# Performance work log

Hardware: AMD Instinct MI355X
Metric: run time of the kernel (lower is better)

## Reference

```python
import jax, jax.numpy as jnp
import numpy as np

S = 2048      # max_seq_len
D_IN = 2048   # input dim
H = 16        # num query heads
KVH = 4       # kv heads (GQA branch)
HD = 128      # per-head embedding dim
D_OUT = 2048
THETA = 10000.0


def rope(x):
    # x: [S, h, d]. Matches eqx.nn.RotaryPositionalEmbedding (GPT-NeoX style):
    # cos/sin of outer(t, inv_freq) tiled over the two halves, rotate_half = (-x2, x1).
    s, h, d = x.shape
    inv_freq = 1.0 / (THETA ** (jnp.arange(0, d, 2, dtype=jnp.float32) / d))  # [d/2]
    t = jnp.arange(s, dtype=jnp.float32)
    freqs = jnp.outer(t, inv_freq)                         # [S, d/2]
    cos = jnp.tile(jnp.cos(freqs), (1, 2))[:, None, :]     # [S, 1, d]
    sin = jnp.tile(jnp.sin(freqs), (1, 2))[:, None, :]
    x1, x2 = jnp.split(x, 2, axis=-1)
    rot = jnp.concatenate((-x2, x1), axis=-1)
    return x * cos + rot * sin


def setup_inputs() -> dict:
    key = jax.random.key(0)
    k0, k1, k2, k3, k4 = jax.random.split(key, 5)
    lim_in = 1.0 / np.sqrt(D_IN).astype(np.float32)
    lim_o = 1.0 / np.sqrt(H * HD).astype(np.float32)
    x = jax.random.normal(k0, (S, D_IN), jnp.float32)
    Wq = jax.random.uniform(k1, (H * HD, D_IN), jnp.float32, -lim_in, lim_in)
    Wk = jax.random.uniform(k2, (KVH * HD, D_IN), jnp.float32, -lim_in, lim_in)
    Wv = jax.random.uniform(k3, (KVH * HD, D_IN), jnp.float32, -lim_in, lim_in)
    Wo = jax.random.uniform(k4, (D_OUT, H * HD), jnp.float32, -lim_o, lim_o)
    return {"x": x, "Wq": Wq, "Wk": Wk, "Wv": Wv, "Wo": Wo}


def reference(x, Wq, Wk, Wv, Wo):
    # Projections (eqx Linear, no bias: y = W @ x)
    q = (x @ Wq.T).reshape(S, H, HD)
    k = (x @ Wk.T).reshape(S, KVH, HD)
    v = (x @ Wv.T).reshape(S, KVH, HD)
    q = rope(q)
    k = rope(k)
    mask = jnp.tril(jnp.ones((S, S), dtype=bool))           # causal
    scale = 1.0 / jnp.sqrt(jnp.asarray(HD, q.dtype))
    # GQA branch: every query head attends against every kv head separately
    logits = jnp.einsum('shd,SHd->hHsS', q * scale, k)      # [H=16, KVH=4, S, S]
    logits = jnp.where(mask, logits, jnp.finfo(logits.dtype).min)
    w = jax.nn.softmax(logits, axis=-1)
    attn = jnp.einsum('hHsS,SHd->shd', w, v) / KVH          # mean over kv heads
    return attn.reshape(S, H * HD) @ Wo.T
```

## Files before the change

### kernel.cpp

```cpp
#include <hip/hip_runtime.h>

#define SEQ 2048
#define DIN 2048
#define NH 16
#define NKVH 4
#define DH 128
#define NQ 2048
#define QSCALE 0.088388347648318447f

typedef unsigned short ushort_t;
typedef unsigned int uint_t;
typedef __attribute__((ext_vector_type(8))) __bf16 bf16x8;
typedef __attribute__((ext_vector_type(8))) unsigned short ushort8;
typedef __attribute__((ext_vector_type(4))) float f32x4;
typedef __attribute__((ext_vector_type(16))) float f32x16;

__device__ __forceinline__ float b2f(ushort_t u){ return __uint_as_float(((unsigned int)u)<<16); }
__device__ __forceinline__ ushort_t f2b(float f){
  unsigned int u = __float_as_uint(f);
  u += 0x7fff + ((u>>16)&1);
  return (ushort_t)(u>>16);
}
__device__ __forceinline__ f32x4 mfma16(bf16x8 a, bf16x8 b, f32x4 c){
  return __builtin_amdgcn_mfma_f32_16x16x32_bf16(a, b, c, 0, 0, 0);
}
__device__ __forceinline__ f32x16 mfma32(bf16x8 a, bf16x8 b, f32x16 c){
  return __builtin_amdgcn_mfma_f32_32x32x16_bf16(a, b, c, 0, 0, 0);
}
__device__ __forceinline__ void gload16(const void* g, void* l){
  __builtin_amdgcn_global_load_lds((__attribute__((address_space(1))) void*)(void*)g,
                                   (__attribute__((address_space(3))) void*)l, 16, 0, 0);
}
__device__ __forceinline__ f32x16 zero16(){
  f32x16 z = {0.f,0.f,0.f,0.f,0.f,0.f,0.f,0.f,0.f,0.f,0.f,0.f,0.f,0.f,0.f,0.f};
  return z;
}

__global__ void detect_bf16(const ushort_t* __restrict__ wq, int* __restrict__ flag){
  __shared__ int any_big;
  if (threadIdx.x==0) any_big = 0;
  __syncthreads();
  int big = 0;
  for (int i=threadIdx.x; i<4096; i+=256){
    float v = b2f(wq[i]);
    if (!(fabsf(v) < 1.0f)) big = 1;
  }
  if (big) atomicOr(&any_big, 1);
  __syncthreads();
  if (threadIdx.x==0) flag[0] = any_big ? 0 : 1;
}

__global__ __launch_bounds__(256)
void cvt_bf16(const void* __restrict__ src, ushort_t* __restrict__ dst,
              const int* __restrict__ flag){
  const int i = (blockIdx.x*256 + threadIdx.x)*8;
  if (flag[0]){
    *(ushort8*)&dst[i] = *(const ushort8*)((const ushort_t*)src + i);
  } else {
    f32x4 a = *(const f32x4*)((const float*)src + i);
    f32x4 b = *(const f32x4*)((const float*)src + i + 4);
    ushort8 w;
    #pragma unroll
    for (int e=0;e<4;e++){ w[e]=f2b(a[e]); w[4+e]=f2b(b[e]); }
    *(ushort8*)&dst[i] = w;
  }
}

__global__ __launch_bounds__(256)
void sum4(const ushort_t* __restrict__ pb, ushort_t* __restrict__ ab){
  const size_t PS = (size_t)SEQ*NQ;
  const int i = (blockIdx.x*256 + threadIdx.x)*8;
  ushort8 a = *(const ushort8*)&pb[i];
  ushort8 b = *(const ushort8*)&pb[PS + i];
  ushort8 c = *(const ushort8*)&pb[2*PS + i];
  ushort8 d = *(const ushort8*)&pb[3*PS + i];
  ushort8 w;
  #pragma unroll
  for (int e=0;e<8;e++)
    w[e] = f2b((b2f(a[e]) + b2f(b[e])) + (b2f(c[e]) + b2f(d[e])));
  *(ushort8*)&ab[i] = w;
}

__device__ __forceinline__ void stage128x32(const ushort_t* src, int ld, char* ldsbase, int tid){
  #pragma unroll
  for (int p=0;p<2;p++){
    int lin = p*4096 + tid*16;
    int r = lin>>6, cb = lin&63;
    gload16(src + (size_t)r*ld + (cb>>1), ldsbase + p*4096 + ((tid>>6)<<10));
  }
}

__global__ __launch_bounds__(256, 2)
void gemm_qkv(const ushort_t* __restrict__ X, const ushort_t* __restrict__ Wq,
              const ushort_t* __restrict__ Wk, const ushort_t* __restrict__ Wv,
              ushort_t* __restrict__ qb, ushort_t* __restrict__ kb,
              ushort_t* __restrict__ vb){
  __shared__ __attribute__((aligned(16))) ushort_t lds_a[2][128*32];
  __shared__ __attribute__((aligned(16))) ushort_t lds_b[2][128*32];
  const int tid = threadIdx.x;
  const int wid = tid>>6, lane = tid&63;
  const int lhi = lane>>4, llo = lane&15;
  const int flat = blockIdx.x + 16*blockIdx.y;
  const int wf = (flat & 7)*48 + (flat >> 3);
  const int mb = (wf & 15)*128;
  const int ny = wf >> 4;
  const ushort_t* W = (ny < 16) ? (Wq + (size_t)ny*128*DIN)
                    : (ny < 20) ? (Wk + (size_t)(ny-16)*128*DIN)
                    : (Wv + (size_t)(ny-20)*128*DIN);
  const int wr = (wid>>1)*64, wc = (wid&1)*64;

  f32x4 acc[4][4];
  #pragma unroll
  for (int i=0;i<4;i++)
    #pragma unroll
    for (int j=0;j<4;j++) acc[i][j] = (f32x4){0.f,0.f,0.f,0.f};

  auto stage = [&](int b, int t){
    stage128x32(X + (size_t)mb*DIN + t*32, DIN, (char*)lds_a[b], tid);
    stage128x32(W + t*32, DIN, (char*)lds_b[b], tid);
  };

  stage(0, 0);
  __syncthreads();
  int cur = 0;
  for (int t=0; t<64; ++t){
    if (t < 63) stage(cur^1, t+1);
    bf16x8 af[4], bfr[4];
    #pragma unroll
    for (int i=0;i<4;i++) af[i]  = *(const bf16x8*)&lds_a[cur][(wr+i*16+llo)*32 + lhi*8];
    #pragma unroll
    for (int j=0;j<4;j++) bfr[j] = *(const bf16x8*)&lds_b[cur][(wc+j*16+llo)*32 + lhi*8];
    __builtin_amdgcn_s_setprio(1);
    #pragma unroll
    for (int i=0;i<4;i++)
      #pragma unroll
      for (int j=0;j<4;j++)
        acc[i][j] = mfma16(af[i], bfr[j], acc[i][j]);
    __builtin_amdgcn_s_setprio(0);
    __syncthreads();
    cur ^= 1;
  }
  #pragma unroll
  for (int i=0;i<4;i++)
    #pragma unroll
    for (int j=0;j<4;j++)
      #pragma unroll
      for (int rr=0;rr<4;rr++){
        int s  = mb + wr + i*16 + lhi*4 + rr;
        int nl = wc + j*16 + llo;
        ushort_t val = f2b(acc[i][j][rr]);
        if (ny < 16)      qb[(size_t)s*NQ + ny*128 + nl] = val;
        else if (ny < 20) kb[(size_t)(ny-16)*SEQ*DH + (size_t)s*DH + nl] = val;
        else              vb[(size_t)(ny-20)*SEQ*DH + (size_t)s*DH + nl] = val;
      }
}

__global__ __launch_bounds__(256, 2)
void gemm_plain_b16(const ushort_t* __restrict__ A, const ushort_t* __restrict__ Wo,
                    void* __restrict__ out, const int* __restrict__ flag){
  __shared__ __attribute__((aligned(16))) ushort_t lds_a[2][128*32];
  __shared__ __attribute__((aligned(16))) ushort_t lds_b[2][128*32];
  const int isb = flag[0];
  const int tid = threadIdx.x;
  const int wid = tid>>6, lane = tid&63;
  const int lhi = lane>>4, llo = lane&15;
  const int flat = blockIdx.x + 16*blockIdx.y;
  const int wf = (flat & 7)*32 + (flat >> 3);
  const int mb = (wf & 15)*128;
  const int nb = (wf >> 4)*128;
  const int wr = (wid>>1)*64, wc = (wid&1)*64;

  f32x4 acc[4][4];
  #pragma unroll
  for (int i=0;i<4;i++)
    #pragma unroll
    for (int j=0;j<4;j++) acc[i][j] = (f32x4){0.f,0.f,0.f,0.f};

  auto stage = [&](int b, int t){
    stage128x32(A  + (size_t)mb*NQ + t*32, NQ, (char*)lds_a[b], tid);
    stage128x32(Wo + (size_t)nb*NQ + t*32, NQ, (char*)lds_b[b], tid);
  };

  stage(0, 0);
  __syncthreads();
  int cur = 0;
  for (int t=0; t<64; ++t){
    if (t < 63) stage(cur^1, t+1);
    bf16x8 af[4], bfr[4];
    #pragma unroll
    for (int i=0;i<4;i++) af[i]  = *(const bf16x8*)&lds_a[cur][(wr+i*16+llo)*32 + lhi*8];
    #pragma unroll
    for (int j=0;j<4;j++) bfr[j] = *(const bf16x8*)&lds_b[cur][(wc+j*16+llo)*32 + lhi*8];
    __builtin_amdgcn_s_setprio(1);
    #pragma unroll
    for (int i=0;i<4;i++)
      #pragma unroll
      for (int j=0;j<4;j++)
        acc[i][j] = mfma16(af[i], bfr[j], acc[i][j]);
    __builtin_amdgcn_s_setprio(0);
    __syncthreads();
    cur ^= 1;
  }
  #pragma unroll
  for (int i=0;i<4;i++)
    #pragma unroll
    for (int j=0;j<4;j++)
      #pragma unroll
      for (int rr=0;rr<4;rr++){
        int s  = mb + wr + i*16 + lhi*4 + rr;
        int nl = nb + wc + j*16 + llo;
        float v = acc[i][j][rr];
        if (isb) ((ushort_t*)out)[(size_t)s*NQ + nl] = f2b(v);
        else     ((float*)out)[(size_t)s*NQ + nl] = v;
      }
}

__global__ __launch_bounds__(256, 2)
void gemm_plain_f32(const float* __restrict__ A, const ushort_t* __restrict__ Wo,
                    void* __restrict__ out, const int* __restrict__ flag){
  __shared__ __attribute__((aligned(16))) ushort_t lds_a[2][128*32];
  __shared__ __attribute__((aligned(16))) ushort_t lds_b[2][128*32];
  const int isb = flag[0];
  const int tid = threadIdx.x;
  const int wid = tid>>6, lane = tid&63;
  const int lhi = lane>>4, llo = lane&15;
  const int mb = blockIdx.x*128;
  const int nb = blockIdx.y*128;
  const int wr = (wid>>1)*64, wc = (wid&1)*64;
  const int r = tid>>1, c0 = (tid&1)*16;
  const float* Ab = A + (size_t)(mb+r)*NQ + c0;

  f32x4 acc[4][4];
  #pragma unroll
  for (int i=0;i<4;i++)
    #pragma unroll
    for (int j=0;j<4;j++) acc[i][j] = (f32x4){0.f,0.f,0.f,0.f};

  f32x4 raf[4];
  auto ldA = [&](int t){
    raf[0] = *(const f32x4*)(Ab + t*32);
    raf[1] = *(const f32x4*)(Ab + t*32 + 4);
    raf[2] = *(const f32x4*)(Ab + t*32 + 8);
    raf[3] = *(const f32x4*)(Ab + t*32 + 12);
  };
  auto stA = [&](ushort_t* lds){
    ushort8 w0, w1;
    #pragma unroll
    for (int e=0;e<4;e++){ w0[e]=f2b(raf[0][e]); w0[4+e]=f2b(raf[1][e]);
                           w1[e]=f2b(raf[2][e]); w1[4+e]=f2b(raf[3][e]); }
    *(ushort8*)&lds[r*32+c0]   = w0;
    *(ushort8*)&lds[r*32+c0+8] = w1;
  };

  ldA(0);
  stage128x32(Wo + (size_t)nb*NQ, NQ, (char*)lds_b[0], tid);
  stA(lds_a[0]);
  __syncthreads();
  int cur = 0;
  for (int t=0; t<64; ++t){
    const bool more = (t < 63);
    if (more){
      ldA(t+1);
      stage128x32(Wo + (size_t)nb*NQ + (t+1)*32, NQ, (char*)lds_b[cur^1], tid);
    }
    bf16x8 af[4], bfr[4];
    #pragma unroll
    for (int i=0;i<4;i++) af[i]  = *(const bf16x8*)&lds_a[cur][(wr+i*16+llo)*32 + lhi*8];
    #pragma unroll
    for (int j=0;j<4;j++) bfr[j] = *(const bf16x8*)&lds_b[cur][(wc+j*16+llo)*32 + lhi*8];
    __builtin_amdgcn_s_setprio(1);
    #pragma unroll
    for (int i=0;i<4;i++)
      #pragma unroll
      for (int j=0;j<4;j++)
        acc[i][j] = mfma16(af[i], bfr[j], acc[i][j]);
    __builtin_amdgcn_s_setprio(0);
    if (more) stA(lds_a[cur^1]);
    __syncthreads();
    cur ^= 1;
  }
  #pragma unroll
  for (int i=0;i<4;i++)
    #pragma unroll
    for (int j=0;j<4;j++)
      #pragma unroll
      for (int rr=0;rr<4;rr++){
        int s  = mb + wr + i*16 + lhi*4 + rr;
        int nl = nb + wc + j*16 + llo;
        float v = acc[i][j][rr];
        if (isb) ((ushort_t*)out)[(size_t)s*NQ + nl] = f2b(v);
        else     ((float*)out)[(size_t)s*NQ + nl] = v;
      }
}

__global__ __launch_bounds__(256)
void rope_kernel(ushort_t* __restrict__ buf, int head_stride, int row_stride, float scale){
  const int idx = blockIdx.x*256 + threadIdx.x;
  const int j = idx & 63;
  const int s = (idx>>6) & (SEQ-1);
  const int h = idx>>17;
  const size_t a1 = (size_t)h*head_stride + (size_t)s*row_stride + j;
  const size_t a2 = a1 + 64;
  const float inv = __expf((float)j * -0.1439115683f);
  const float ang = (float)s * inv;
  const float c = cosf(ang), sn = sinf(ang);
  const float x1 = b2f(buf[a1]), x2 = b2f(buf[a2]);
  buf[a1] = f2b((x1*c - x2*sn)*scale);
  buf[a2] = f2b((x2*c + x1*sn)*scale);
}

__global__ __launch_bounds__(256)
void vtrans(const ushort_t* __restrict__ vb, ushort_t* __restrict__ vt){
  __shared__ __attribute__((aligned(16))) ushort_t tile[64*72];
  const int tid = threadIdx.x;
  const int kv = blockIdx.z, s0 = blockIdx.x*64, d0 = blockIdx.y*64;
  #pragma unroll
  for (int p=0;p<2;p++){
    int lin = p*4096 + tid*16;
    int rr = lin>>7, cb = lin&127;
    ushort8 val = *(const ushort8*)&vb[(size_t)kv*SEQ*DH + (size_t)(s0+rr)*DH + d0 + (cb>>1)];
    *(ushort8*)&tile[rr*72 + (cb>>1)] = val;
  }
  __syncthreads();
  #pragma unroll
  for (int p=0;p<2;p++){
    int lin = p*4096 + tid*16;
    int rr = lin>>7, cb = lin&127;
    int cc = cb>>1;
    ushort8 val;
    #pragma unroll
    for (int e=0;e<8;e++) val[e] = tile[(cc+e)*72 + rr];
    *(ushort8*)&vt[(size_t)kv*DH*SEQ + (size_t)(d0+rr)*SEQ + s0 + cc] = val;
  }
}

__global__ __launch_bounds__(256, 2)
void attn_kernel(const ushort_t* __restrict__ qb, const ushort_t* __restrict__ kb,
                 const ushort_t* __restrict__ vt, float* __restrict__ abf,
                 ushort_t* __restrict__ pb, int use_pb){
  __shared__ __attribute__((aligned(16))) ushort_t lds_k[2][64*128];
  __shared__ __attribute__((aligned(16))) ushort_t lds_v[2][128*64];
  __shared__ float lsum[4][32];
  const int tid = threadIdx.x;
  const int wid = tid>>6, lane = tid&63;
  const int l31 = lane&31, hi = lane>>5;
  const int flat = (int)(blockIdx.x + 8*blockIdx.y + 128*blockIdx.z);
  const int xcd = flat & 7, slot = flat >> 3;
  const int kv = xcd >> 1;
  const int ph = (xcd & 1)*64 + slot;
  const int p = ph & 7, h = ph >> 3;
  const ushort_t* kbase = kb + (size_t)kv*SEQ*DH;
  const ushort_t* vbase = vt + (size_t)kv*DH*SEQ;
  const int NKT0 = 2*p + 2;

  auto stage = [&](int b, int kt){
    #pragma unroll
    for (int pp=0;pp<4;pp++){
      int lin = pp*4096 + tid*16;
      int rk = lin>>8, cbk = lin&255;
      int sck = cbk ^ ((rk&15)<<4);
      gload16(kbase + (size_t)(kt*64 + rk)*DH + (sck>>1), (char*)lds_k[b] + pp*4096 + (wid<<10));
      int rv = lin>>7, cbv = lin&127;
      int scv = cbv ^ ((rv&7)<<4);
      gload16(vbase + (size_t)rv*SEQ + kt*64 + (scv>>1), (char*)lds_v[b] + pp*4096 + (wid<<10));
    }
  };

  int sub = 0, kt = 0, t = p;
  int qrow0 = t*128 + wid*32;
  int qg = qrow0 + l31;
  bf16x8 qf[8];
  {
    const ushort_t* qp = qb + (size_t)qg*NQ + h*DH + hi*8;
    #pragma unroll
    for (int ks=0;ks<8;ks++) qf[ks] = *(const bf16x8*)(qp + ks*16);
  }
  f32x16 oacc[4];
  #pragma unroll
  for (int d=0;d<4;d++) oacc[d] = zero16();
  float psum = 0.f;

  stage(0, 0);
  __syncthreads();
  int cur = 0;

  for (int s=0; s<34; ++s){
    {
      int ns = s + 1;
      if (ns < 34) stage(cur^1, ns < NKT0 ? ns : ns - NKT0);
    }
    #pragma unroll
    for (int ss=0;ss<2;ss++){
      const int kvb = kt*64 + ss*32;
      if (kvb > qrow0 + 31) continue;
      f32x16 sacc = zero16();
      #pragma unroll
      for (int ks=0;ks<8;ks++){
        int row = ss*32 + l31;
        int boff = row*256 + ((ks*32 + hi*16) ^ ((row&15)<<4));
        bf16x8 kf = *(const bf16x8*)((const char*)lds_k[cur] + boff);
        sacc = mfma32(kf, qf[ks], sacc);
      }
      const bool edge = (kvb + 31 > qrow0);
      #pragma unroll
      for (int rr=0; rr<16; rr++){
        float e = __expf(sacc[rr]);
        if (edge){
          int kvg = kvb + (rr&3) + 8*(rr>>2) + 4*hi;
          if (kvg > qg) e = 0.f;
        }
        sacc[rr] = e;
        psum += e;
      }
      #pragma unroll
      for (int pk=0; pk<2; pk++){
        uint_t P0, P1, P2, P3;
        asm("v_cvt_pk_bf16_f32 %0, %1, %2" : "=v"(P0) : "v"(sacc[8*pk+0]), "v"(sacc[8*pk+1]));
        asm("v_cvt_pk_bf16_f32 %0, %1, %2" : "=v"(P1) : "v"(sacc[8*pk+2]), "v"(sacc[8*pk+3]));
        asm("v_cvt_pk_bf16_f32 %0, %1, %2" : "=v"(P2) : "v"(sacc[8*pk+4]), "v"(sacc[8*pk+5]));
        asm("v_cvt_pk_bf16_f32 %0, %1, %2" : "=v"(P3) : "v"(sacc[8*pk+6]), "v"(sacc[8*pk+7]));
        asm("v_permlane32_swap_b32 %0, %1" : "+v"(P0), "+v"(P2));
        asm("v_permlane32_swap_b32 %0, %1" : "+v"(P1), "+v"(P3));
        uint4 fu; fu.x = P0; fu.y = P1; fu.z = P2; fu.w = P3;
        bf16x8 pf = *(bf16x8*)&fu;
        #pragma unroll
        for (int d=0; d<4; d++){
          int rowv = d*32 + l31;
          int bv = rowv*128 + ((ss*64 + pk*32 + hi*16) ^ ((rowv&7)<<4));
          bf16x8 vf = *(const bf16x8*)((const char*)lds_v[cur] + bv);
          oacc[d] = mfma32(pf, vf, oacc[d]);
        }
      }
    }
    const int NKTc = sub ? (34 - NKT0) : NKT0;
    if (kt == NKTc - 1){
      float tot = psum + __shfl_xor(psum, 32);
      lsum[wid][l31] = tot;
      if (use_pb){
        ushort_t* pbk = pb + (size_t)kv*SEQ*NQ + (size_t)h*DH;
        #pragma unroll
        for (int rr=0; rr<16; rr++){
          int qr = (rr&3) + 8*(rr>>2) + 4*hi;
          float sc = 0.25f / lsum[wid][qr];
          #pragma unroll
          for (int d=0; d<4; d++)
            pbk[(size_t)(qrow0 + qr)*NQ + d*32 + l31] = f2b(oacc[d][rr]*sc);
        }
      } else {
        #pragma unroll
        for (int rr=0; rr<16; rr++){
          int qr = (rr&3) + 8*(rr>>2) + 4*hi;
          float sc = 0.25f / lsum[wid][qr];
          #pragma unroll
          for (int d=0; d<4; d++)
            atomicAdd(&abf[(size_t)(qrow0 + qr)*NQ + h*DH + d*32 + l31], oacc[d][rr]*sc);
        }
      }
      if (sub == 0){
        sub = 1; kt = 0; t = 15 - p;
        qrow0 = t*128 + wid*32; qg = qrow0 + l31;
        const ushort_t* qp = qb + (size_t)qg*NQ + h*DH + hi*8;
        #pragma unroll
        for (int ks=0;ks<8;ks++) qf[ks] = *(const bf16x8*)(qp + ks*16);
        #pragma unroll
        for (int d=0;d<4;d++) oacc[d] = zero16();
        psum = 0.f;
      }
    } else {
      kt++;
    }
    __syncthreads();
    cur ^= 1;
  }
}

extern "C" void kernel_launch(void* const* d_in, const int* in_sizes, int n_in,
                              void* d_out, int out_size, void* d_ws, size_t ws_size,
                              hipStream_t stream) {
  const void* x  = d_in[0];
  const void* wq = d_in[1];
  const void* wk = d_in[2];
  const void* wv = d_in[3];
  const void* wo = d_in[4];
  char* ws = (char*)d_ws;
  const bool big_ws = (ws_size >= ((size_t)55<<20));

  if (big_ws){
    ushort_t* qbuf = (ushort_t*)(ws);
    ushort_t* kbuf = (ushort_t*)(ws + ((size_t)8<<20));
    ushort_t* vbuf = (ushort_t*)(ws + ((size_t)10<<20));
    ushort_t* vtb  = (ushort_t*)(ws + ((size_t)12<<20));
    ushort_t* pbuf = (ushort_t*)(ws + ((size_t)14<<20));
    ushort_t* xb   = (ushort_t*)(ws + ((size_t)14<<20));
    ushort_t* wqb  = (ushort_t*)(ws + ((size_t)22<<20));
    ushort_t* wkb  = (ushort_t*)(ws + ((size_t)30<<20));
    ushort_t* wvb  = (ushort_t*)(ws + ((size_t)32<<20));
    ushort_t* wob  = (ushort_t*)(ws + ((size_t)46<<20));
    ushort_t* ab   = qbuf;
    int* flag      = (int*)(ws + ((size_t)54<<20));

    hipLaunchKernelGGL(detect_bf16, dim3(1), dim3(256), 0, stream, (const ushort_t*)wq, flag);
    hipLaunchKernelGGL(cvt_bf16, dim3(2048), dim3(256), 0, stream, x,  xb,  flag);
    hipLaunchKernelGGL(cvt_bf16, dim3(2048), dim3(256), 0, stream, wq, wqb, flag);
    hipLaunchKernelGGL(cvt_bf16, dim3(512),  dim3(256), 0, stream, wk, wkb, flag);
    hipLaunchKernelGGL(cvt_bf16, dim3(512),  dim3(256), 0, stream, wv, wvb, flag);
    hipLaunchKernelGGL(cvt_bf16, dim3(2048), dim3(256), 0, stream, wo, wob, flag);
    hipLaunchKernelGGL(gemm_qkv, dim3(16,24), dim3(256), 0, stream, xb, wqb, wkb, wvb, qbuf, kbuf, vbuf);
    hipLaunchKernelGGL(rope_kernel, dim3(8192), dim3(256), 0, stream, qbuf, DH, NQ, QSCALE);
    hipLaunchKernelGGL(rope_kernel, dim3(2048), dim3(256), 0, stream, kbuf, SEQ*DH, DH, 1.0f);
    hipLaunchKernelGGL(vtrans, dim3(32,2,4), dim3(256), 0, stream, vbuf, vtb);
    hipLaunchKernelGGL(attn_kernel, dim3(8,16,4), dim3(256), 0, stream, qbuf, kbuf, vtb,
                       (float*)nullptr, pbuf, 1);
    hipLaunchKernelGGL(sum4, dim3(2048), dim3(256), 0, stream, pbuf, ab);
    hipLaunchKernelGGL(gemm_plain_b16, dim3(16,16), dim3(256), 0, stream, ab, wob, d_out, flag);
  } else {
    ushort_t* qbuf = (ushort_t*)(ws);
    ushort_t* kbuf = (ushort_t*)(ws + ((size_t)8<<20));
    ushort_t* vbuf = (ushort_t*)(ws + ((size_t)10<<20));
    ushort_t* vtb  = (ushort_t*)(ws + ((size_t)12<<20));
    float*    abf  = (float*)(ws + ((size_t)14<<20));
    ushort_t* xb   = (ushort_t*)(ws + ((size_t)14<<20));
    ushort_t* wqb  = (ushort_t*)(ws + ((size_t)22<<20));
    ushort_t* wkb  = (ushort_t*)(ws + ((size_t)30<<20));
    ushort_t* wvb  = (ushort_t*)(ws + ((size_t)32<<20));
    ushort_t* wob  = (ushort_t*)(ws + ((size_t)34<<20));
    int* flag      = (int*)(ws + ((size_t)42<<20));

    hipLaunchKernelGGL(detect_bf16, dim3(1), dim3(256), 0, stream, (const ushort_t*)wq, flag);
    hipLaunchKernelGGL(cvt_bf16, dim3(2048), dim3(256), 0, stream, x,  xb,  flag);
    hipLaunchKernelGGL(cvt_bf16, dim3(2048), dim3(256), 0, stream, wq, wqb, flag);
    hipLaunchKernelGGL(cvt_bf16, dim3(512),  dim3(256), 0, stream, wk, wkb, flag);
    hipLaunchKernelGGL(cvt_bf16, dim3(512),  dim3(256), 0, stream, wv, wvb, flag);
    hipLaunchKernelGGL(cvt_bf16, dim3(2048), dim3(256), 0, stream, wo, wob, flag);
    hipLaunchKernelGGL(gemm_qkv, dim3(16,24), dim3(256), 0, stream, xb, wqb, wkb, wvb, qbuf, kbuf, vbuf);
    hipMemsetAsync(abf, 0, (size_t)SEQ*NQ*sizeof(float), stream);
    hipLaunchKernelGGL(rope_kernel, dim3(8192), dim3(256), 0, stream, qbuf, DH, NQ, QSCALE);
    hipLaunchKernelGGL(rope_kernel, dim3(2048), dim3(256), 0, stream, kbuf, SEQ*DH, DH, 1.0f);
    hipLaunchKernelGGL(vtrans, dim3(32,2,4), dim3(256), 0, stream, vbuf, vtb);
    hipLaunchKernelGGL(attn_kernel, dim3(8,16,4), dim3(256), 0, stream, qbuf, kbuf, vtb,
                       abf, (ushort_t*)nullptr, 0);
    hipLaunchKernelGGL(gemm_plain_f32, dim3(16,16), dim3(256), 0, stream, abf, wob, d_out, flag);
  }
}
```

Baseline: 219.0 us.

## Fuse conversion and rope launches, shrink GEMM tiles, simplify attention to one tile per block

Folds the five conversion launches into one cvt_all kernel and the two rope launches into one rope_all, which cuts launch overhead. Halves the GEMM tile in one dimension (QKV uses 64x128, the output projection 128x64) so more blocks fill the CUs, and raises QKV occupancy to 3 blocks per CU. The attention kernel drops the paired-tile double-buffered pipeline for one query tile per block with single-buffered LDS, ordered to balance causal work, at 4 blocks per CU. It also folds log2(e) into the Q scale so exp2 can replace expf. These changes trade lost load/compute overlap in attention and less per-block reuse in the GEMMs for more parallelism and fewer launches.

```diff
diff --git a/kernel.cpp b/kernel.cpp
--- a/kernel.cpp
+++ b/kernel.cpp
@@ -6,7 +6,7 @@
 #define NKVH 4
 #define DH 128
 #define NQ 2048
-#define QSCALE 0.088388347648318447f
+#define QSCALE2 0.1275174684f
 
 typedef unsigned short ushort_t;
 typedef unsigned int uint_t;
@@ -14,6 +14,12 @@
 typedef __attribute__((ext_vector_type(8))) unsigned short ushort8;
 typedef __attribute__((ext_vector_type(4))) float f32x4;
 typedef __attribute__((ext_vector_type(16))) float f32x16;
+
+#if __has_builtin(__builtin_amdgcn_exp2f)
+#define EXP2(x) __builtin_amdgcn_exp2f(x)
+#else
+#define EXP2(x) exp2f(x)
+#endif
 
 __device__ __forceinline__ float b2f(ushort_t u){ return __uint_as_float(((unsigned int)u)<<16); }
 __device__ __forceinline__ ushort_t f2b(float f){
@@ -51,17 +57,28 @@
 }
 
 __global__ __launch_bounds__(256)
-void cvt_bf16(const void* __restrict__ src, ushort_t* __restrict__ dst,
-              const int* __restrict__ flag){
-  const int i = (blockIdx.x*256 + threadIdx.x)*8;
+void cvt_all(const void* __restrict__ x, const void* __restrict__ wq,
+             const void* __restrict__ wk, const void* __restrict__ wv,
+             const void* __restrict__ wo,
+             ushort_t* __restrict__ xb, ushort_t* __restrict__ wqb,
+             ushort_t* __restrict__ wkb, ushort_t* __restrict__ wvb,
+             ushort_t* __restrict__ wob, const int* __restrict__ flag){
+  int b = blockIdx.x;
+  const void* src; ushort_t* dst; int off;
+  if      (b < 2048){ src=x;  dst=xb;  off=b; }
+  else if (b < 4096){ src=wq; dst=wqb; off=b-2048; }
+  else if (b < 4608){ src=wk; dst=wkb; off=b-4096; }
+  else if (b < 5120){ src=wv; dst=wvb; off=b-4608; }
+  else              { src=wo; dst=wob; off=b-5120; }
+  const int i = (off*256 + threadIdx.x)*8;
   if (flag[0]){
     *(ushort8*)&dst[i] = *(const ushort8*)((const ushort_t*)src + i);
   } else {
     f32x4 a = *(const f32x4*)((const float*)src + i);
-    f32x4 b = *(const f32x4*)((const float*)src + i + 4);
+    f32x4 c = *(const f32x4*)((const float*)src + i + 4);
     ushort8 w;
     #pragma unroll
-    for (int e=0;e<4;e++){ w[e]=f2b(a[e]); w[4+e]=f2b(b[e]); }
+    for (int e=0;e<4;e++){ w[e]=f2b(a[e]); w[4+e]=f2b(c[e]); }
     *(ushort8*)&dst[i] = w;
   }
 }
@@ -89,34 +106,39 @@
     gload16(src + (size_t)r*ld + (cb>>1), ldsbase + p*4096 + ((tid>>6)<<10));
   }
 }
-
-__global__ __launch_bounds__(256, 2)
+__device__ __forceinline__ void stage64x32(const ushort_t* src, int ld, char* ldsbase, int tid){
+  int lin = tid*16;
+  int r = lin>>6, cb = lin&63;
+  gload16(src + (size_t)r*ld + (cb>>1), ldsbase + ((tid>>6)<<10));
+}
+
+__global__ __launch_bounds__(256, 3)
 void gemm_qkv(const ushort_t* __restrict__ X, const ushort_t* __restrict__ Wq,
               const ushort_t* __restrict__ Wk, const ushort_t* __restrict__ Wv,
               ushort_t* __restrict__ qb, ushort_t* __restrict__ kb,
               ushort_t* __restrict__ vb){
-  __shared__ __attribute__((aligned(16))) ushort_t lds_a[2][128*32];
+  __shared__ __attribute__((aligned(16))) ushort_t lds_a[2][64*32];
   __shared__ __attribute__((aligned(16))) ushort_t lds_b[2][128*32];
   const int tid = threadIdx.x;
   const int wid = tid>>6, lane = tid&63;
   const int lhi = lane>>4, llo = lane&15;
-  const int flat = blockIdx.x + 16*blockIdx.y;
-  const int wf = (flat & 7)*48 + (flat >> 3);
-  const int mb = (wf & 15)*128;
-  const int ny = wf >> 4;
+  const int flat = blockIdx.x;
+  const int wf = (flat & 7)*96 + (flat >> 3);
+  const int mb = (wf & 31)*64;
+  const int ny = wf >> 5;
   const ushort_t* W = (ny < 16) ? (Wq + (size_t)ny*128*DIN)
                     : (ny < 20) ? (Wk + (size_t)(ny-16)*128*DIN)
                     : (Wv + (size_t)(ny-20)*128*DIN);
-  const int wr = (wid>>1)*64, wc = (wid&1)*64;
-
-  f32x4 acc[4][4];
-  #pragma unroll
-  for (int i=0;i<4;i++)
+  const int wr = (wid>>1)*32, wc = (wid&1)*64;
+
+  f32x4 acc[2][4];
+  #pragma unroll
+  for (int i=0;i<2;i++)
     #pragma unroll
     for (int j=0;j<4;j++) acc[i][j] = (f32x4){0.f,0.f,0.f,0.f};
 
   auto stage = [&](int b, int t){
-    stage128x32(X + (size_t)mb*DIN + t*32, DIN, (char*)lds_a[b], tid);
+    stage64x32 (X + (size_t)mb*DIN + t*32, DIN, (char*)lds_a[b], tid);
     stage128x32(W + t*32, DIN, (char*)lds_b[b], tid);
   };
 
@@ -125,14 +147,14 @@
   int cur = 0;
   for (int t=0; t<64; ++t){
     if (t < 63) stage(cur^1, t+1);
-    bf16x8 af[4], bfr[4];
-    #pragma unroll
-    for (int i=0;i<4;i++) af[i]  = *(const bf16x8*)&lds_a[cur][(wr+i*16+llo)*32 + lhi*8];
+    bf16x8 af[2], bfr[4];
+    #pragma unroll
+    for (int i=0;i<2;i++) af[i]  = *(const bf16x8*)&lds_a[cur][(wr+i*16+llo)*32 + lhi*8];
     #pragma unroll
     for (int j=0;j<4;j++) bfr[j] = *(const bf16x8*)&lds_b[cur][(wc+j*16+llo)*32 + lhi*8];
     __builtin_amdgcn_s_setprio(1);
     #pragma unroll
-    for (int i=0;i<4;i++)
+    for (int i=0;i<2;i++)
       #pragma unroll
       for (int j=0;j<4;j++)
         acc[i][j] = mfma16(af[i], bfr[j], acc[i][j]);
@@ -141,7 +163,7 @@
     cur ^= 1;
   }
   #pragma unroll
-  for (int i=0;i<4;i++)
+  for (int i=0;i<2;i++)
     #pragma unroll
     for (int j=0;j<4;j++)
       #pragma unroll
@@ -159,26 +181,26 @@
 void gemm_plain_b16(const ushort_t* __restrict__ A, const ushort_t* __restrict__ Wo,
                     void* __restrict__ out, const int* __restrict__ flag){
   __shared__ __attribute__((aligned(16))) ushort_t lds_a[2][128*32];
-  __shared__ __attribute__((aligned(16))) ushort_t lds_b[2][128*32];
+  __shared__ __attribute__((aligned(16))) ushort_t lds_b[2][64*32];
   const int isb = flag[0];
   const int tid = threadIdx.x;
   const int wid = tid>>6, lane = tid&63;
   const int lhi = lane>>4, llo = lane&15;
-  const int flat = blockIdx.x + 16*blockIdx.y;
-  const int wf = (flat & 7)*32 + (flat >> 3);
+  const int flat = blockIdx.x;
+  const int wf = (flat & 7)*64 + (flat >> 3);
   const int mb = (wf & 15)*128;
-  const int nb = (wf >> 4)*128;
-  const int wr = (wid>>1)*64, wc = (wid&1)*64;
-
-  f32x4 acc[4][4];
+  const int nb = (wf >> 4)*64;
+  const int wr = (wid>>1)*64, wc = (wid&1)*32;
+
+  f32x4 acc[4][2];
   #pragma unroll
   for (int i=0;i<4;i++)
     #pragma unroll
-    for (int j=0;j<4;j++) acc[i][j] = (f32x4){0.f,0.f,0.f,0.f};
+    for (int j=0;j<2;j++) acc[i][j] = (f32x4){0.f,0.f,0.f,0.f};
 
   auto stage = [&](int b, int t){
     stage128x32(A  + (size_t)mb*NQ + t*32, NQ, (char*)lds_a[b], tid);
-    stage128x32(Wo + (size_t)nb*NQ + t*32, NQ, (char*)lds_b[b], tid);
+    stage64x32 (Wo + (size_t)nb*NQ + t*32, NQ, (char*)lds_b[b], tid);
   };
 
   stage(0, 0);
@@ -186,16 +208,16 @@
   int cur = 0;
   for (int t=0; t<64; ++t){
     if (t < 63) stage(cur^1, t+1);
-    bf16x8 af[4], bfr[4];
+    bf16x8 af[4], bfr[2];
     #pragma unroll
     for (int i=0;i<4;i++) af[i]  = *(const bf16x8*)&lds_a[cur][(wr+i*16+llo)*32 + lhi*8];
     #pragma unroll
-    for (int j=0;j<4;j++) bfr[j] = *(const bf16x8*)&lds_b[cur][(wc+j*16+llo)*32 + lhi*8];
+    for (int j=0;j<2;j++) bfr[j] = *(const bf16x8*)&lds_b[cur][(wc+j*16+llo)*32 + lhi*8];
     __builtin_amdgcn_s_setprio(1);
     #pragma unroll
     for (int i=0;i<4;i++)
       #pragma unroll
-      for (int j=0;j<4;j++)
+      for (int j=0;j<2;j++)
         acc[i][j] = mfma16(af[i], bfr[j], acc[i][j]);
     __builtin_amdgcn_s_setprio(0);
     __syncthreads();
@@ -204,7 +226,7 @@
   #pragma unroll
   for (int i=0;i<4;i++)
     #pragma unroll
-    for (int j=0;j<4;j++)
+    for (int j=0;j<2;j++)
       #pragma unroll
       for (int rr=0;rr<4;rr++){
         int s  = mb + wr + i*16 + lhi*4 + rr;
@@ -294,8 +316,11 @@
 }
 
 __global__ __launch_bounds__(256)
-void rope_kernel(ushort_t* __restrict__ buf, int head_stride, int row_stride, float scale){
-  const int idx = blockIdx.x*256 + threadIdx.x;
+void rope_all(ushort_t* __restrict__ qbuf, ushort_t* __restrict__ kbuf){
+  int idx = blockIdx.x*256 + threadIdx.x;
+  ushort_t* buf; int head_stride, row_stride; float scale;
+  if (idx < 16*SEQ*64){ buf=qbuf; head_stride=DH; row_stride=NQ; scale=QSCALE2; }
+  else { idx -= 16*SEQ*64; buf=kbuf; head_stride=SEQ*DH; row_stride=DH; scale=1.0f; }
   const int j = idx & 63;
   const int s = (idx>>6) & (SEQ-1);
   const int h = idx>>17;
@@ -334,61 +359,53 @@
   }
 }
 
-__global__ __launch_bounds__(256, 2)
+__global__ __launch_bounds__(256, 4)
 void attn_kernel(const ushort_t* __restrict__ qb, const ushort_t* __restrict__ kb,
                  const ushort_t* __restrict__ vt, float* __restrict__ abf,
                  ushort_t* __restrict__ pb, int use_pb){
-  __shared__ __attribute__((aligned(16))) ushort_t lds_k[2][64*128];
-  __shared__ __attribute__((aligned(16))) ushort_t lds_v[2][128*64];
+  __shared__ __attribute__((aligned(16))) ushort_t lds_k[64*128];
+  __shared__ __attribute__((aligned(16))) ushort_t lds_v[128*64];
   __shared__ float lsum[4][32];
   const int tid = threadIdx.x;
   const int wid = tid>>6, lane = tid&63;
   const int l31 = lane&31, hi = lane>>5;
-  const int flat = (int)(blockIdx.x + 8*blockIdx.y + 128*blockIdx.z);
+  const int flat = (int)(blockIdx.x + 16*blockIdx.y + 256*blockIdx.z);
   const int xcd = flat & 7, slot = flat >> 3;
   const int kv = xcd >> 1;
-  const int ph = (xcd & 1)*64 + slot;
-  const int p = ph & 7, h = ph >> 3;
+  const int idx = slot*2 + (xcd & 1);
+  const int g = idx >> 4, h = idx & 15;
+  const int t = (g<4) ? 15-g : (g<8) ? 4+g : (g<12) ? g-4 : 15-g;
   const ushort_t* kbase = kb + (size_t)kv*SEQ*DH;
   const ushort_t* vbase = vt + (size_t)kv*DH*SEQ;
-  const int NKT0 = 2*p + 2;
-
-  auto stage = [&](int b, int kt){
+  const int NKT = 2*t + 2;
+  const int qrow0 = t*128 + wid*32;
+  const int qg = qrow0 + l31;
+
+  bf16x8 qf[8];
+  {
+    const ushort_t* qp = qb + (size_t)qg*NQ + h*DH + hi*8;
+    #pragma unroll
+    for (int ks=0;ks<8;ks++) qf[ks] = *(const bf16x8*)(qp + ks*16);
+  }
+  f32x16 oacc[4];
+  #pragma unroll
+  for (int d=0;d<4;d++) oacc[d] = zero16();
+  float psum = 0.f;
+
+  for (int kt=0; kt<NKT; ++kt){
+    __syncthreads();
     #pragma unroll
     for (int pp=0;pp<4;pp++){
       int lin = pp*4096 + tid*16;
       int rk = lin>>8, cbk = lin&255;
       int sck = cbk ^ ((rk&15)<<4);
-      gload16(kbase + (size_t)(kt*64 + rk)*DH + (sck>>1), (char*)lds_k[b] + pp*4096 + (wid<<10));
+      gload16(kbase + (size_t)(kt*64 + rk)*DH + (sck>>1), (char*)lds_k + pp*4096 + (wid<<10));
       int rv = lin>>7, cbv = lin&127;
       int scv = cbv ^ ((rv&7)<<4);
-      gload16(vbase + (size_t)rv*SEQ + kt*64 + (scv>>1), (char*)lds_v[b] + pp*4096 + (wid<<10));
+      gload16(vbase + (size_t)rv*SEQ + kt*64 + (scv>>1), (char*)lds_v + pp*4096 + (wid<<10));
     }
-  };
-
-  int sub = 0, kt = 0, t = p;
-  int qrow0 = t*128 + wid*32;
-  int qg = qrow0 + l31;
-  bf16x8 qf[8];
-  {
-    const ushort_t* qp = qb + (size_t)qg*NQ + h*DH + hi*8;
-    #pragma unroll
-    for (int ks=0;ks<8;ks++) qf[ks] = *(const bf16x8*)(qp + ks*16);
-  }
-  f32x16 oacc[4];
-  #pragma unroll
-  for (int d=0;d<4;d++) oacc[d] = zero16();
-  float psum = 0.f;
-
-  stage(0, 0);
-  __syncthreads();
-  int cur = 0;
-
-  for (int s=0; s<34; ++s){
-    {
-      int ns = s + 1;
-      if (ns < 34) stage(cur^1, ns < NKT0 ? ns : ns - NKT0);
-    }
+    __syncthreads();
+
     #pragma unroll
     for (int ss=0;ss<2;ss++){
       const int kvb = kt*64 + ss*32;
@@ -398,13 +415,13 @@
       for (int ks=0;ks<8;ks++){
         int row = ss*32 + l31;
         int boff = row*256 + ((ks*32 + hi*16) ^ ((row&15)<<4));
-        bf16x8 kf = *(const bf16x8*)((const char*)lds_k[cur] + boff);
+        bf16x8 kf = *(const bf16x8*)((const char*)lds_k + boff);
         sacc = mfma32(kf, qf[ks], sacc);
       }
       const bool edge = (kvb + 31 > qrow0);
       #pragma unroll
       for (int rr=0; rr<16; rr++){
-        float e = __expf(sacc[rr]);
+        float e = EXP2(sacc[rr]);
         if (edge){
           int kvg = kvb + (rr&3) + 8*(rr>>2) + 4*hi;
           if (kvg > qg) e = 0.f;
@@ -427,50 +444,36 @@
         for (int d=0; d<4; d++){
           int rowv = d*32 + l31;
           int bv = rowv*128 + ((ss*64 + pk*32 + hi*16) ^ ((rowv&7)<<4));
-          bf16x8 vf = *(const bf16x8*)((const char*)lds_v[cur] + bv);
+          bf16x8 vf = *(const bf16x8*)((const char*)lds_v + bv);
           oacc[d] = mfma32(pf, vf, oacc[d]);
         }
       }
     }
-    const int NKTc = sub ? (34 - NKT0) : NKT0;
-    if (kt == NKTc - 1){
-      float tot = psum + __shfl_xor(psum, 32);
-      lsum[wid][l31] = tot;
-      if (use_pb){
-        ushort_t* pbk = pb + (size_t)kv*SEQ*NQ + (size_t)h*DH;
+  }
+
+  {
+    float tot = psum + __shfl_xor(psum, 32);
+    lsum[wid][l31] = tot;
+    if (use_pb){
+      ushort_t* pbk = pb + (size_t)kv*SEQ*NQ + (size_t)h*DH;
+      #pragma unroll
+      for (int rr=0; rr<16; rr++){
+        int qr = (rr&3) + 8*(rr>>2) + 4*hi;
+        float sc = 0.25f / lsum[wid][qr];
         #pragma unroll
-        for (int rr=0; rr<16; rr++){
-          int qr = (rr&3) + 8*(rr>>2) + 4*hi;
-          float sc = 0.25f / lsum[wid][qr];
-          #pragma unroll
-          for (int d=0; d<4; d++)
-            pbk[(size_t)(qrow0 + qr)*NQ + d*32 + l31] = f2b(oacc[d][rr]*sc);
-        }
-      } else {
+        for (int d=0; d<4; d++)
+          pbk[(size_t)(qrow0 + qr)*NQ + d*32 + l31] = f2b(oacc[d][rr]*sc);
+      }
+    } else {
+      #pragma unroll
+      for (int rr=0; rr<16; rr++){
+        int qr = (rr&3) + 8*(rr>>2) + 4*hi;
+        float sc = 0.25f / lsum[wid][qr];
         #pragma unroll
-        for (int rr=0; rr<16; rr++){
-          int qr = (rr&3) + 8*(rr>>2) + 4*hi;
-          float sc = 0.25f / lsum[wid][qr];
-          #pragma unroll
-          for (int d=0; d<4; d++)
-            atomicAdd(&abf[(size_t)(qrow0 + qr)*NQ + h*DH + d*32 + l31], oacc[d][rr]*sc);
-        }
-      }
-      if (sub == 0){
-        sub = 1; kt = 0; t = 15 - p;
-        qrow0 = t*128 + wid*32; qg = qrow0 + l31;
-        const ushort_t* qp = qb + (size_t)qg*NQ + h*DH + hi*8;
-        #pragma unroll
-        for (int ks=0;ks<8;ks++) qf[ks] = *(const bf16x8*)(qp + ks*16);
-        #pragma unroll
-        for (int d=0;d<4;d++) oacc[d] = zero16();
-        psum = 0.f;
-      }
-    } else {
-      kt++;
+        for (int d=0; d<4; d++)
+          atomicAdd(&abf[(size_t)(qrow0 + qr)*NQ + h*DH + d*32 + l31], oacc[d][rr]*sc);
+      }
     }
-    __syncthreads();
-    cur ^= 1;
   }
 }
 
@@ -500,19 +503,15 @@
     int* flag      = (int*)(ws + ((size_t)54<<20));
 
     hipLaunchKernelGGL(detect_bf16, dim3(1), dim3(256), 0, stream, (const ushort_t*)wq, flag);
-    hipLaunchKernelGGL(cvt_bf16, dim3(2048), dim3(256), 0, stream, x,  xb,  flag);
-    hipLaunchKernelGGL(cvt_bf16, dim3(2048), dim3(256), 0, stream, wq, wqb, flag);
-    hipLaunchKernelGGL(cvt_bf16, dim3(512),  dim3(256), 0, stream, wk, wkb, flag);
-    hipLaunchKernelGGL(cvt_bf16, dim3(512),  dim3(256), 0, stream, wv, wvb, flag);
-    hipLaunchKernelGGL(cvt_bf16, dim3(2048), dim3(256), 0, stream, wo, wob, flag);
-    hipLaunchKernelGGL(gemm_qkv, dim3(16,24), dim3(256), 0, stream, xb, wqb, wkb, wvb, qbuf, kbuf, vbuf);
-    hipLaunchKernelGGL(rope_kernel, dim3(8192), dim3(256), 0, stream, qbuf, DH, NQ, QSCALE);
-    hipLaunchKernelGGL(rope_kernel, dim3(2048), dim3(256), 0, stream, kbuf, SEQ*DH, DH, 1.0f);
+    hipLaunchKernelGGL(cvt_all, dim3(7168), dim3(256), 0, stream, x, wq, wk, wv, wo,
+                       xb, wqb, wkb, wvb, wob, flag);
+    hipLaunchKernelGGL(gemm_qkv, dim3(768), dim3(256), 0, stream, xb, wqb, wkb, wvb, qbuf, kbuf, vbuf);
+    hipLaunchKernelGGL(rope_all, dim3(10240), dim3(256), 0, stream, qbuf, kbuf);
     hipLaunchKernelGGL(vtrans, dim3(32,2,4), dim3(256), 0, stream, vbuf, vtb);
-    hipLaunchKernelGGL(attn_kernel, dim3(8,16,4), dim3(256), 0, stream, qbuf, kbuf, vtb,
+    hipLaunchKernelGGL(attn_kernel, dim3(16,16,4), dim3(256), 0, stream, qbuf, kbuf, vtb,
                        (float*)nullptr, pbuf, 1);
     hipLaunchKernelGGL(sum4, dim3(2048), dim3(256), 0, stream, pbuf, ab);
-    hipLaunchKernelGGL(gemm_plain_b16, dim3(16,16), dim3(256), 0, stream, ab, wob, d_out, flag);
+    hipLaunchKernelGGL(gemm_plain_b16, dim3(512), dim3(256), 0, stream, ab, wob, d_out, flag);
   } else {
     ushort_t* qbuf = (ushort_t*)(ws);
     ushort_t* kbuf = (ushort_t*)(ws + ((size_t)8<<20));
@@ -527,17 +526,13 @@
     int* flag      = (int*)(ws + ((size_t)42<<20));
 
     hipLaunchKernelGGL(detect_bf16, dim3(1), dim3(256), 0, stream, (const ushort_t*)wq, flag);
-    hipLaunchKernelGGL(cvt_bf16, dim3(2048), dim3(256), 0, stream, x,  xb,  flag);
-    hipLaunchKernelGGL(cvt_bf16, dim3(2048), dim3(256), 0, stream, wq, wqb, flag);
-    hipLaunchKernelGGL(cvt_bf16, dim3(512),  dim3(256), 0, stream, wk, wkb, flag);
-    hipLaunchKernelGGL(cvt_bf16, dim3(512),  dim3(256), 0, stream, wv, wvb, flag);
-    hipLaunchKernelGGL(cvt_bf16, dim3(2048), dim3(256), 0, stream, wo, wob, flag);
-    hipLaunchKernelGGL(gemm_qkv, dim3(16,24), dim3(256), 0, stream, xb, wqb, wkb, wvb, qbuf, kbuf, vbuf);
+    hipLaunchKernelGGL(cvt_all, dim3(7168), dim3(256), 0, stream, x, wq, wk, wv, wo,
+                       xb, wqb, wkb, wvb, wob, flag);
+    hipLaunchKernelGGL(gemm_qkv, dim3(768), dim3(256), 0, stream, xb, wqb, wkb, wvb, qbuf, kbuf, vbuf);
     hipMemsetAsync(abf, 0, (size_t)SEQ*NQ*sizeof(float), stream);
-    hipLaunchKernelGGL(rope_kernel, dim3(8192), dim3(256), 0, stream, qbuf, DH, NQ, QSCALE);
-    hipLaunchKernelGGL(rope_kernel, dim3(2048), dim3(256), 0, stream, kbuf, SEQ*DH, DH, 1.0f);
+    hipLaunchKernelGGL(rope_all, dim3(10240), dim3(256), 0, stream, qbuf, kbuf);
     hipLaunchKernelGGL(vtrans, dim3(32,2,4), dim3(256), 0, stream, vbuf, vtb);
-    hipLaunchKernelGGL(attn_kernel, dim3(8,16,4), dim3(256), 0, stream, qbuf, kbuf, vtb,
+    hipLaunchKernelGGL(attn_kernel, dim3(16,16,4), dim3(256), 0, stream, qbuf, kbuf, vtb,
                        abf, (ushort_t*)nullptr, 0);
     hipLaunchKernelGGL(gemm_plain_f32, dim3(16,16), dim3(256), 0, stream, abf, wob, d_out, flag);
   }
```

Result: slower. 344.2 us (+57.2%).
